# Kernel tuning notes

Measured on AMD Instinct MI355X. Metric: run time of the kernel, lower is better.

## Reference

```python
import jax, jax.numpy as jnp
import numpy as np

N, E = 10000, 320000
IN, H, C, ED = 256, 4, 64, 64
HC = H * C
EPS = 1e-5
NEG_SLOPE = 0.2


def setup_inputs() -> dict:
    key = jax.random.key(0)
    ks = jax.random.split(key, 12)
    g = lambda k, shape, fan: jax.random.normal(k, shape, jnp.float32) * (1.0 / np.sqrt(fan))
    return {
        "x": jax.random.normal(ks[0], (N, IN), jnp.float32),
        "edge_index": jax.random.randint(ks[1], (2, E), 0, N, jnp.int64),
        "edge_attr": jax.random.normal(ks[2], (E, ED), jnp.float32),
        "Wl": g(ks[3], (HC, IN), IN),   # lin_l weight (source)
        "bl": jnp.zeros((HC,), jnp.float32),
        "Wr": g(ks[4], (HC, IN), IN),   # lin_r weight (target)
        "br": jnp.zeros((HC,), jnp.float32),
        "We": g(ks[5], (HC, ED), ED),   # lin_edge weight (no bias)
        "att": g(ks[6], (H, C), C),
        "bias": jnp.zeros((HC,), jnp.float32),
        "gamma": jnp.ones((HC,), jnp.float32),
        "beta": jnp.zeros((HC,), jnp.float32),
    }


def reference(x, edge_index, edge_attr, Wl, bl, Wr, br, We, att, bias, gamma, beta):
    src, dst = edge_index[0], edge_index[1]
    # add_self_loops with fill_value='mean': loop edge_attr = mean of incoming attrs
    ones = jnp.ones((E,), jnp.float32)
    cnt = jax.ops.segment_sum(ones, dst, num_segments=N)              # [N]
    loop_attr = jax.ops.segment_sum(edge_attr, dst, num_segments=N) / jnp.maximum(cnt, 1.0)[:, None]
    node_ids = jnp.arange(N, dtype=src.dtype)
    src_f = jnp.concatenate([src, node_ids])                          # [E+N]
    dst_f = jnp.concatenate([dst, node_ids])
    ea = jnp.concatenate([edge_attr, loop_attr], axis=0)              # [E+N, ED]

    xl = (x @ Wl.T + bl).reshape(N, H, C)   # source-side projection
    xr = (x @ Wr.T + br).reshape(N, H, C)   # target-side projection
    ep = (ea @ We.T).reshape(-1, H, C)       # edge projection

    m = xl[src_f] + xr[dst_f] + ep                                    # [E+N, H, C]
    m = jnp.where(m >= 0, m, NEG_SLOPE * m)                           # leaky_relu(0.2)
    logits = jnp.einsum("ehc,hc->eh", m, att)                        # [E+N, H]

    # segment softmax over target node dst_f (every node has a self loop)
    mx = jax.ops.segment_max(logits, dst_f, num_segments=N)
    ex = jnp.exp(logits - mx[dst_f])
    den = jax.ops.segment_sum(ex, dst_f, num_segments=N)
    alpha = ex / den[dst_f]                                           # [E+N, H]

    out = jax.ops.segment_sum(xl[src_f] * alpha[:, :, None], dst_f, num_segments=N)
    h = out.reshape(N, HC) + bias

    # SiLU then LayerNorm, dropout is identity in eval
    h = h * jax.nn.sigmoid(h)
    mu = jnp.mean(h, axis=-1, keepdims=True)
    var = jnp.mean((h - mu) ** 2, axis=-1, keepdims=True)
    h = (h - mu) * jax.lax.rsqrt(var + EPS) * gamma + beta
    return h, alpha
```

## Files before the change

### kernel.cpp

```cpp
#include <hip/hip_runtime.h>

#define N_NODES 10000
#define N_EDGES 320000
#define NE_TOT  330000
#define NEG_SLOPE 0.2f
#define LN_EPS 1e-5f

#define OFF_CNT    0u
#define OFF_FILL   40000u
#define OFF_ROWPTR 80128u
#define OFF_EIDS   120320u
#define OFF_POSE   1440512u
#define OFF_XLH    4000512u
#define OFF_XRH    9120512u
#define OFF_LOG    14240512u
#define OFF_WLF    19520512u
#define OFF_WRF    19651584u
#define OFF_WEF    19782656u
#define OFF_SD     19815424u
#define OFF_EAC    21135424u

typedef __bf16 bf16x8 __attribute__((ext_vector_type(8)));
typedef float  f32x4  __attribute__((ext_vector_type(4)));
typedef unsigned short us4 __attribute__((ext_vector_type(4)));

__device__ __forceinline__ float bf2f(unsigned short u) {
    union { unsigned int i; float f; } v;
    v.i = ((unsigned int)u) << 16;
    return v.f;
}
__device__ __forceinline__ float lo2f(unsigned int u) {
    union { unsigned int i; float f; } v;
    v.i = u << 16;
    return v.f;
}
__device__ __forceinline__ float hi2f(unsigned int u) {
    union { unsigned int i; float f; } v;
    v.i = u & 0xFFFF0000u;
    return v.f;
}
__device__ __forceinline__ unsigned short f2bf(float x) {
    __bf16 b = (__bf16)x;
    return __builtin_bit_cast(unsigned short, b);
}
__device__ __forceinline__ bf16x8 cvt8(const float* p) {
    float4 v0 = *reinterpret_cast<const float4*>(p);
    float4 v1 = *reinterpret_cast<const float4*>(p + 4);
    bf16x8 t;
    t[0] = (__bf16)v0.x; t[1] = (__bf16)v0.y; t[2] = (__bf16)v0.z; t[3] = (__bf16)v0.w;
    t[4] = (__bf16)v1.x; t[5] = (__bf16)v1.y; t[6] = (__bf16)v1.z; t[7] = (__bf16)v1.w;
    return t;
}

__global__ void k_count(const int* __restrict__ ei, int* __restrict__ cnt) {
    int e = blockIdx.x * blockDim.x + threadIdx.x;
    if (e < N_EDGES) atomicAdd(&cnt[ei[N_EDGES + e]], 1);
}

__global__ void k_scan(const int* __restrict__ cnt, int* __restrict__ row_ptr) {
    __shared__ int sums[1024];
    int t = threadIdx.x;
    const int CH = 10;
    int base = t * CH;
    int s = 0;
    for (int i = 0; i < CH; i++) {
        int n = base + i;
        if (n < N_NODES) s += cnt[n] + 1;
    }
    sums[t] = s;
    __syncthreads();
    for (int off = 1; off < 1024; off <<= 1) {
        int v = (t >= off) ? sums[t - off] : 0;
        __syncthreads();
        sums[t] += v;
        __syncthreads();
    }
    int run = (t == 0) ? 0 : sums[t - 1];
    for (int i = 0; i < CH; i++) {
        int n = base + i;
        if (n < N_NODES) { row_ptr[n] = run; run += cnt[n] + 1; }
    }
    if (t == 1023) row_ptr[N_NODES] = sums[1023];
}

__global__ void k_fill(const int* __restrict__ ei, const int* __restrict__ row_ptr,
                       int* __restrict__ fill, int* __restrict__ eids,
                       int* __restrict__ sdv, int* __restrict__ pose) {
    int e = blockIdx.x * blockDim.x + threadIdx.x;
    if (e >= NE_TOT) return;
    int s, d;
    if (e < N_EDGES) { s = ei[e]; d = ei[N_EDGES + e]; }
    else             { s = e - N_EDGES; d = s; }
    int pos = atomicAdd(&fill[d], 1);
    int p = row_ptr[d] + pos;
    eids[p] = e;
    sdv[p] = s | (d << 16);
    pose[e] = p;
}

__global__ void k_permute_e(const float* __restrict__ edge_attr,
                            const int* __restrict__ pose,
                            unsigned short* __restrict__ eac) {
    int idx = blockIdx.x * blockDim.x + threadIdx.x;
    if (idx >= N_EDGES * 32) return;
    int e = idx >> 5, cp = idx & 31;
    float2 v = reinterpret_cast<const float2*>(edge_attr)[(size_t)e * 32 + cp];
    int p = pose[e];
    unsigned int u = ((unsigned int)f2bf(v.x)) | (((unsigned int)f2bf(v.y)) << 16);
    reinterpret_cast<unsigned int*>(eac)[(size_t)p * 32 + cp] = u;
}

__global__ void k_self_attr(const int* __restrict__ row_ptr,
                            const int* __restrict__ pose,
                            unsigned short* __restrict__ eac) {
    int node = (blockIdx.x << 2) + (threadIdx.x >> 6);
    int lane = threadIdx.x & 63;
    int b = row_ptr[node], en = row_ptr[node + 1];
    int selfp = pose[N_EDGES + node];
    float s0 = 0.0f, s1 = 0.0f;
    int i = b;
    for (; i + 1 < en; i += 2) {
        float a0 = bf2f(eac[(size_t)(i + 0) * 64 + lane]);
        float a1 = bf2f(eac[(size_t)(i + 1) * 64 + lane]);
        s0 += (i + 0 == selfp) ? 0.0f : a0;
        s1 += (i + 1 == selfp) ? 0.0f : a1;
    }
    for (; i < en; i++) {
        float a = bf2f(eac[(size_t)i * 64 + lane]);
        s0 += (i == selfp) ? 0.0f : a;
    }
    float s = s0 + s1;
    float c = (float)(en - b - 1);
    eac[(size_t)selfp * 64 + lane] = f2bf(s / fmaxf(c, 1.0f));
}

__global__ void k_prep_wfrag(const float* __restrict__ Wl,
                             const float* __restrict__ Wr,
                             const float* __restrict__ We,
                             unsigned short* __restrict__ wlf,
                             unsigned short* __restrict__ wrf,
                             unsigned short* __restrict__ wef) {
    int idx = blockIdx.x * 256 + threadIdx.x;
    if (idx >= 8192) return;
    int ln = idx & 63;
    int ts = (idx >> 6) & 7;
    int ct = idx >> 9;
    int c = ct * 16 + (ln & 15);
    int k0 = ts * 32 + (ln >> 4) * 8;
    *reinterpret_cast<bf16x8*>(wlf + (size_t)idx * 8) = cvt8(Wl + (size_t)c * 256 + k0);
    *reinterpret_cast<bf16x8*>(wrf + (size_t)idx * 8) = cvt8(Wr + (size_t)c * 256 + k0);
    if (idx < 2048) {
        int f = idx >> 6;
        int cb = f >> 1, step = f & 1;
        int ce = cb * 16 + (ln & 15);
        int ke = step * 32 + (ln >> 4) * 8;
        *reinterpret_cast<bf16x8*>(wef + (size_t)idx * 8) = cvt8(We + (size_t)ce * 64 + ke);
    }
}

__global__ __launch_bounds__(256) void k_gemm_mfma(
        const float* __restrict__ x,
        const float* __restrict__ bl, const float* __restrict__ br,
        const unsigned short* __restrict__ wlf,
        const unsigned short* __restrict__ wrf,
        unsigned short* __restrict__ xlh,
        unsigned short* __restrict__ xrh) {
    __shared__ __bf16 xs[8 * 64 * 8];
    int tid = threadIdx.x;
    int nb = blockIdx.x * 16;

    for (int f = tid; f < 512; f += 256) {
        int t = f >> 6, ln = f & 63;
        int node = nb + (ln & 15);
        int k0 = t * 32 + (ln >> 4) * 8;
        *reinterpret_cast<bf16x8*>(&xs[f * 8]) = cvt8(x + (size_t)node * 256 + k0);
    }
    __syncthreads();

    int lane = tid & 63;
    int wv = tid >> 6;
    int quad = lane >> 4;
    int ln15 = lane & 15;

    bf16x8 bfr[8];
#pragma unroll
    for (int t = 0; t < 8; t++)
        bfr[t] = *reinterpret_cast<const bf16x8*>(&xs[(t * 64 + lane) * 8]);

    int node = nb + ln15;
#pragma unroll
    for (int ci = 0; ci < 4; ci++) {
        int ct = wv * 4 + ci;
        f32x4 accl, accr;
        accl[0] = accl[1] = accl[2] = accl[3] = 0.0f;
        accr[0] = accr[1] = accr[2] = accr[3] = 0.0f;
#pragma unroll
        for (int t = 0; t < 8; t++) {
            bf16x8 al = *reinterpret_cast<const bf16x8*>(
                wlf + ((size_t)(ct * 8 + t) * 64 + lane) * 8);
            accl = __builtin_amdgcn_mfma_f32_16x16x32_bf16(al, bfr[t], accl, 0, 0, 0);
        }
#pragma unroll
        for (int t = 0; t < 8; t++) {
            bf16x8 ar = *reinterpret_cast<const bf16x8*>(
                wrf + ((size_t)(ct * 8 + t) * 64 + lane) * 8);
            accr = __builtin_amdgcn_mfma_f32_16x16x32_bf16(ar, bfr[t], accr, 0, 0, 0);
        }
        int cbase = ct * 16 + quad * 4;
        float4 blv = *reinterpret_cast<const float4*>(bl + cbase);
        float4 brv = *reinterpret_cast<const float4*>(br + cbase);
        us4 ol, orr;
        ol[0] = f2bf(accl[0] + blv.x); ol[1] = f2bf(accl[1] + blv.y);
        ol[2] = f2bf(accl[2] + blv.z); ol[3] = f2bf(accl[3] + blv.w);
        orr[0] = f2bf(accr[0] + brv.x); orr[1] = f2bf(accr[1] + brv.y);
        orr[2] = f2bf(accr[2] + brv.z); orr[3] = f2bf(accr[3] + brv.w);
        *reinterpret_cast<us4*>(xlh + (size_t)node * 256 + cbase) = ol;
        *reinterpret_cast<us4*>(xrh + (size_t)node * 256 + cbase) = orr;
    }
}

__global__ __launch_bounds__(256) void k_logits_v2(
        const int* __restrict__ sdv,
        const unsigned short* __restrict__ eac,
        const unsigned short* __restrict__ wef,
        const unsigned short* __restrict__ xlh,
        const unsigned short* __restrict__ xrh,
        const float* __restrict__ att,
        float* __restrict__ logits) {
    __shared__ unsigned short ep_s[4][4096];
    int tid = threadIdx.x;
    int wv = tid >> 6, lane = tid & 63;
    int h = lane >> 4, l15 = lane & 15;
    unsigned short* eps = ep_s[wv];

    const uint2* xl2 = reinterpret_cast<const uint2*>(xlh);
    const uint2* xr2 = reinterpret_cast<const uint2*>(xrh);
    float4 atv = reinterpret_cast<const float4*>(att)[lane];

    int wswz = (l15 & 3) << 4;

    const int ntiles = NE_TOT / 16;
#pragma unroll 1
    for (int t = blockIdx.x * 4 + wv; t < ntiles; t += gridDim.x * 4) {
        int pos0 = t * 16;
        int sdl = sdv[pos0 + l15];

        const unsigned short* row = eac + (size_t)(pos0 + l15) * 64;
        bf16x8 b0 = *reinterpret_cast<const bf16x8*>(row + h * 8);
        bf16x8 b1 = *reinterpret_cast<const bf16x8*>(row + 32 + h * 8);
#pragma unroll
        for (int cb = 0; cb < 16; cb++) {
            f32x4 acc;
            acc[0] = acc[1] = acc[2] = acc[3] = 0.0f;
            bf16x8 a0 = *reinterpret_cast<const bf16x8*>(
                wef + ((size_t)(cb * 2 + 0) * 64 + lane) * 8);
            bf16x8 a1 = *reinterpret_cast<const bf16x8*>(
                wef + ((size_t)(cb * 2 + 1) * 64 + lane) * 8);
            acc = __builtin_amdgcn_mfma_f32_16x16x32_bf16(a0, b0, acc, 0, 0, 0);
            acc = __builtin_amdgcn_mfma_f32_16x16x32_bf16(a1, b1, acc, 0, 0, 0);
            us4 o;
            o[0] = f2bf(acc[0]); o[1] = f2bf(acc[1]);
            o[2] = f2bf(acc[2]); o[3] = f2bf(acc[3]);
            *reinterpret_cast<us4*>(&eps[l15 * 256 + ((cb * 16 + h * 4) ^ wswz)]) = o;
        }

#pragma unroll 4
        for (int j = 0; j < 16; j++) {
            int pos = pos0 + j;
            int sd = __shfl(sdl, j, 64);
            int s = sd & 0xFFFF;
            int d = sd >> 16;
            uint2 xlv = xl2[(size_t)s * 64 + lane];
            uint2 xrv = xr2[(size_t)d * 64 + lane];
            us4 epv = *reinterpret_cast<const us4*>(
                &eps[j * 256 + ((lane * 4) ^ ((j & 3) << 4))]);
            float v0 = lo2f(xlv.x) + lo2f(xrv.x) + bf2f(epv[0]);
            v0 = fmaxf(v0, NEG_SLOPE * v0);
            float v1 = hi2f(xlv.x) + hi2f(xrv.x) + bf2f(epv[1]);
            v1 = fmaxf(v1, NEG_SLOPE * v1);
            float v2 = lo2f(xlv.y) + lo2f(xrv.y) + bf2f(epv[2]);
            v2 = fmaxf(v2, NEG_SLOPE * v2);
            float v3 = hi2f(xlv.y) + hi2f(xrv.y) + bf2f(epv[3]);
            v3 = fmaxf(v3, NEG_SLOPE * v3);
            float hs = fmaf(v0, atv.x, fmaf(v1, atv.y, fmaf(v2, atv.z, v3 * atv.w)));
            hs += __shfl_xor(hs, 1, 64);
            hs += __shfl_xor(hs, 2, 64);
            hs += __shfl_xor(hs, 4, 64);
            hs += __shfl_xor(hs, 8, 64);
            if (l15 == 0) logits[(size_t)pos * 4 + h] = hs;
        }
    }
}

__global__ void k_aggregate(const int* __restrict__ sdv,
                            const int* __restrict__ row_ptr,
                            const int* __restrict__ eids,
                            const float* __restrict__ logits,
                            const unsigned short* __restrict__ xlh,
                            const float* __restrict__ bias,
                            const float* __restrict__ gamma,
                            const float* __restrict__ beta,
                            float* __restrict__ hout,
                            float* __restrict__ alpha_out) {
    int node = (blockIdx.x << 2) + (threadIdx.x >> 6);
    int lane = threadIdx.x & 63;
    int h = lane >> 4;
    int b = row_ptr[node], en = row_ptr[node + 1];
    const uint2* xl2 = reinterpret_cast<const uint2*>(xlh);

    float m0 = -INFINITY, m1 = -INFINITY, m2 = -INFINITY, m3 = -INFINITY;
    int i = b;
    for (; i + 3 < en; i += 4) {
        m0 = fmaxf(m0, logits[(i + 0) * 4 + h]);
        m1 = fmaxf(m1, logits[(i + 1) * 4 + h]);
        m2 = fmaxf(m2, logits[(i + 2) * 4 + h]);
        m3 = fmaxf(m3, logits[(i + 3) * 4 + h]);
    }
    for (; i < en; i++) m0 = fmaxf(m0, logits[i * 4 + h]);
    float mh = fmaxf(fmaxf(m0, m1), fmaxf(m2, m3));

    float d0 = 0.0f, d1 = 0.0f, d2 = 0.0f, d3 = 0.0f;
    i = b;
    for (; i + 3 < en; i += 4) {
        d0 += __expf(logits[(i + 0) * 4 + h] - mh);
        d1 += __expf(logits[(i + 1) * 4 + h] - mh);
        d2 += __expf(logits[(i + 2) * 4 + h] - mh);
        d3 += __expf(logits[(i + 3) * 4 + h] - mh);
    }
    for (; i < en; i++) d0 += __expf(logits[i * 4 + h] - mh);
    float rden = 1.0f / ((d0 + d1) + (d2 + d3));

    float4 ac0; ac0.x = ac0.y = ac0.z = ac0.w = 0.0f;
    float4 ac1; ac1.x = ac1.y = ac1.z = ac1.w = 0.0f;
    i = b;
    for (; i + 3 < en; i += 4) {
        int sd0 = sdv[i + 0], sd1 = sdv[i + 1], sd2 = sdv[i + 2], sd3 = sdv[i + 3];
        float lg0 = logits[(i + 0) * 4 + h], lg1 = logits[(i + 1) * 4 + h];
        float lg2 = logits[(i + 2) * 4 + h], lg3 = logits[(i + 3) * 4 + h];
        int e0 = eids[i + 0], e1 = eids[i + 1], e2 = eids[i + 2], e3 = eids[i + 3];
        uint2 x0 = xl2[(size_t)(sd0 & 0xFFFF) * 64 + lane];
        uint2 x1 = xl2[(size_t)(sd1 & 0xFFFF) * 64 + lane];
        uint2 x2 = xl2[(size_t)(sd2 & 0xFFFF) * 64 + lane];
        uint2 x3 = xl2[(size_t)(sd3 & 0xFFFF) * 64 + lane];
        float al0 = __expf(lg0 - mh) * rden;
        float al1 = __expf(lg1 - mh) * rden;
        float al2 = __expf(lg2 - mh) * rden;
        float al3 = __expf(lg3 - mh) * rden;
        if ((lane & 15) == 0) {
            alpha_out[e0 * 4 + h] = al0; alpha_out[e1 * 4 + h] = al1;
            alpha_out[e2 * 4 + h] = al2; alpha_out[e3 * 4 + h] = al3;
        }
        ac0.x = fmaf(al0, lo2f(x0.x), ac0.x); ac0.y = fmaf(al0, hi2f(x0.x), ac0.y);
        ac0.z = fmaf(al0, lo2f(x0.y), ac0.z); ac0.w = fmaf(al0, hi2f(x0.y), ac0.w);
        ac1.x = fmaf(al1, lo2f(x1.x), ac1.x); ac1.y = fmaf(al1, hi2f(x1.x), ac1.y);
        ac1.z = fmaf(al1, lo2f(x1.y), ac1.z); ac1.w = fmaf(al1, hi2f(x1.y), ac1.w);
        ac0.x = fmaf(al2, lo2f(x2.x), ac0.x); ac0.y = fmaf(al2, hi2f(x2.x), ac0.y);
        ac0.z = fmaf(al2, lo2f(x2.y), ac0.z); ac0.w = fmaf(al2, hi2f(x2.y), ac0.w);
        ac1.x = fmaf(al3, lo2f(x3.x), ac1.x); ac1.y = fmaf(al3, hi2f(x3.x), ac1.y);
        ac1.z = fmaf(al3, lo2f(x3.y), ac1.z); ac1.w = fmaf(al3, hi2f(x3.y), ac1.w);
    }
    for (; i < en; i++) {
        int e = eids[i];
        int s = sdv[i] & 0xFFFF;
        float al = __expf(logits[i * 4 + h] - mh) * rden;
        if ((lane & 15) == 0) alpha_out[e * 4 + h] = al;
        uint2 xv = xl2[(size_t)s * 64 + lane];
        ac0.x = fmaf(al, lo2f(xv.x), ac0.x); ac0.y = fmaf(al, hi2f(xv.x), ac0.y);
        ac0.z = fmaf(al, lo2f(xv.y), ac0.z); ac0.w = fmaf(al, hi2f(xv.y), ac0.w);
    }
    float4 acc;
    acc.x = ac0.x + ac1.x;
    acc.y = ac0.y + ac1.y;
    acc.z = ac0.z + ac1.z;
    acc.w = ac0.w + ac1.w;

    const float4 b4 = reinterpret_cast<const float4*>(bias)[lane];
    float4 hv;
    hv.x = acc.x + b4.x; hv.y = acc.y + b4.y;
    hv.z = acc.z + b4.z; hv.w = acc.w + b4.w;
    hv.x = hv.x / (1.0f + __expf(-hv.x));
    hv.y = hv.y / (1.0f + __expf(-hv.y));
    hv.z = hv.z / (1.0f + __expf(-hv.z));
    hv.w = hv.w / (1.0f + __expf(-hv.w));
    float s1 = hv.x + hv.y + hv.z + hv.w;
    float s2 = hv.x * hv.x + hv.y * hv.y + hv.z * hv.z + hv.w * hv.w;
#pragma unroll
    for (int off = 1; off < 64; off <<= 1) {
        s1 += __shfl_xor(s1, off, 64);
        s2 += __shfl_xor(s2, off, 64);
    }
    float mu = s1 * (1.0f / 256.0f);
    float var = s2 * (1.0f / 256.0f) - mu * mu;
    float rs = rsqrtf(var + LN_EPS);
    const float4 g4 = reinterpret_cast<const float4*>(gamma)[lane];
    const float4 be4 = reinterpret_cast<const float4*>(beta)[lane];
    float4 o;
    o.x = (hv.x - mu) * rs * g4.x + be4.x;
    o.y = (hv.y - mu) * rs * g4.y + be4.y;
    o.z = (hv.z - mu) * rs * g4.z + be4.z;
    o.w = (hv.w - mu) * rs * g4.w + be4.w;
    reinterpret_cast<float4*>(hout)[node * 64 + lane] = o;
}

extern "C" void kernel_launch(void* const* d_in, const int* in_sizes, int n_in,
                              void* d_out, int out_size, void* d_ws, size_t ws_size,
                              hipStream_t stream) {
    (void)in_sizes; (void)n_in; (void)out_size; (void)ws_size;
    const float* x         = (const float*)d_in[0];
    const int*   ei        = (const int*)d_in[1];
    const float* edge_attr = (const float*)d_in[2];
    const float* Wl        = (const float*)d_in[3];
    const float* bl        = (const float*)d_in[4];
    const float* Wr        = (const float*)d_in[5];
    const float* br        = (const float*)d_in[6];
    const float* We        = (const float*)d_in[7];
    const float* att       = (const float*)d_in[8];
    const float* bias      = (const float*)d_in[9];
    const float* gamma     = (const float*)d_in[10];
    const float* beta      = (const float*)d_in[11];

    char* ws = (char*)d_ws;
    int*   cnt     = (int*)(ws + OFF_CNT);
    int*   fill    = (int*)(ws + OFF_FILL);
    int*   row_ptr = (int*)(ws + OFF_ROWPTR);
    int*   eids    = (int*)(ws + OFF_EIDS);
    int*   pose    = (int*)(ws + OFF_POSE);
    unsigned short* xlh = (unsigned short*)(ws + OFF_XLH);
    unsigned short* xrh = (unsigned short*)(ws + OFF_XRH);
    float* logits  = (float*)(ws + OFF_LOG);
    unsigned short* wlf = (unsigned short*)(ws + OFF_WLF);
    unsigned short* wrf = (unsigned short*)(ws + OFF_WRF);
    unsigned short* wef = (unsigned short*)(ws + OFF_WEF);
    int*   sdv     = (int*)(ws + OFF_SD);
    unsigned short* eac = (unsigned short*)(ws + OFF_EAC);

    float* hout      = (float*)d_out;
    float* alpha_out = (float*)d_out + N_NODES * 256;

    hipMemsetAsync(ws + OFF_CNT, 0, 2 * N_NODES * sizeof(int), stream);

    k_count<<<(N_EDGES + 255) / 256, 256, 0, stream>>>(ei, cnt);
    k_scan<<<1, 1024, 0, stream>>>(cnt, row_ptr);
    k_prep_wfrag<<<32, 256, 0, stream>>>(Wl, Wr, We, wlf, wrf, wef);
    k_fill<<<(NE_TOT + 255) / 256, 256, 0, stream>>>(ei, row_ptr, fill, eids, sdv, pose);
    k_gemm_mfma<<<N_NODES / 16, 256, 0, stream>>>(x, bl, br, wlf, wrf, xlh, xrh);
    k_permute_e<<<(N_EDGES * 32) / 256, 256, 0, stream>>>(edge_attr, pose, eac);
    k_self_attr<<<N_NODES / 4, 256, 0, stream>>>(row_ptr, pose, eac);
    k_logits_v2<<<1024, 256, 0, stream>>>(sdv, eac, wef, xlh, xrh, att, logits);
    k_aggregate<<<N_NODES / 4, 256, 0, stream>>>(sdv, row_ptr, eids, logits, xlh,
                                                 bias, gamma, beta, hout, alpha_out);
}
```

Baseline: 400.8 us.

## Fuse weight prep into count kernel, stage edge weights in LDS, unroll aggregation

Merges the weight-fragment conversion kernel into the edge-count kernel to save a launch. The logits kernel now copies the edge-projection weight fragments and attention vector into shared memory, adjusts the LDS swizzle to cut bank conflicts, and launches twice as many blocks. The aggregation loop is unrolled from 4 to 8 edges, with empty asm barriers that force the gathers to be issued before use. The larger LDS footprint (about 65KB per block) may lower occupancy of the logits kernel.

```diff
diff --git a/kernel.cpp b/kernel.cpp
--- a/kernel.cpp
+++ b/kernel.cpp
@@ -52,9 +52,33 @@
     return t;
 }
 
-__global__ void k_count(const int* __restrict__ ei, int* __restrict__ cnt) {
-    int e = blockIdx.x * blockDim.x + threadIdx.x;
-    if (e < N_EDGES) atomicAdd(&cnt[ei[N_EDGES + e]], 1);
+__global__ void k_pre(const int* __restrict__ ei, int* __restrict__ cnt,
+                      const float* __restrict__ Wl, const float* __restrict__ Wr,
+                      const float* __restrict__ We,
+                      unsigned short* __restrict__ wlf,
+                      unsigned short* __restrict__ wrf,
+                      unsigned short* __restrict__ wef) {
+    int gid = blockIdx.x * 256 + threadIdx.x;
+    if (gid < 8192) {
+        int idx = gid;
+        int ln = idx & 63;
+        int ts = (idx >> 6) & 7;
+        int ct = idx >> 9;
+        int c = ct * 16 + (ln & 15);
+        int k0 = ts * 32 + (ln >> 4) * 8;
+        *reinterpret_cast<bf16x8*>(wlf + (size_t)idx * 8) = cvt8(Wl + (size_t)c * 256 + k0);
+        *reinterpret_cast<bf16x8*>(wrf + (size_t)idx * 8) = cvt8(Wr + (size_t)c * 256 + k0);
+        if (idx < 2048) {
+            int f = idx >> 6;
+            int cb = f >> 1, step = f & 1;
+            int ce = cb * 16 + (ln & 15);
+            int ke = step * 32 + (ln >> 4) * 8;
+            *reinterpret_cast<bf16x8*>(wef + (size_t)idx * 8) = cvt8(We + (size_t)ce * 64 + ke);
+        }
+    } else {
+        int e = gid - 8192;
+        if (e < N_EDGES) atomicAdd(&cnt[ei[N_EDGES + e]], 1);
+    }
 }
 
 __global__ void k_scan(const int* __restrict__ cnt, int* __restrict__ row_ptr) {
@@ -134,30 +158,6 @@
     eac[(size_t)selfp * 64 + lane] = f2bf(s / fmaxf(c, 1.0f));
 }
 
-__global__ void k_prep_wfrag(const float* __restrict__ Wl,
-                             const float* __restrict__ Wr,
-                             const float* __restrict__ We,
-                             unsigned short* __restrict__ wlf,
-                             unsigned short* __restrict__ wrf,
-                             unsigned short* __restrict__ wef) {
-    int idx = blockIdx.x * 256 + threadIdx.x;
-    if (idx >= 8192) return;
-    int ln = idx & 63;
-    int ts = (idx >> 6) & 7;
-    int ct = idx >> 9;
-    int c = ct * 16 + (ln & 15);
-    int k0 = ts * 32 + (ln >> 4) * 8;
-    *reinterpret_cast<bf16x8*>(wlf + (size_t)idx * 8) = cvt8(Wl + (size_t)c * 256 + k0);
-    *reinterpret_cast<bf16x8*>(wrf + (size_t)idx * 8) = cvt8(Wr + (size_t)c * 256 + k0);
-    if (idx < 2048) {
-        int f = idx >> 6;
-        int cb = f >> 1, step = f & 1;
-        int ce = cb * 16 + (ln & 15);
-        int ke = step * 32 + (ln >> 4) * 8;
-        *reinterpret_cast<bf16x8*>(wef + (size_t)idx * 8) = cvt8(We + (size_t)ce * 64 + ke);
-    }
-}
-
 __global__ __launch_bounds__(256) void k_gemm_mfma(
         const float* __restrict__ x,
         const float* __restrict__ bl, const float* __restrict__ br,
@@ -219,7 +219,7 @@
     }
 }
 
-__global__ __launch_bounds__(256) void k_logits_v2(
+__global__ __launch_bounds__(256) void k_logits_v3(
         const int* __restrict__ sdv,
         const unsigned short* __restrict__ eac,
         const unsigned short* __restrict__ wef,
@@ -227,17 +227,29 @@
         const unsigned short* __restrict__ xrh,
         const float* __restrict__ att,
         float* __restrict__ logits) {
+    __shared__ __bf16 wef_s[2048 * 8];
     __shared__ unsigned short ep_s[4][4096];
+    __shared__ float att_s[256];
     int tid = threadIdx.x;
+    for (int f = tid; f < 2048; f += 256) {
+        *reinterpret_cast<bf16x8*>(&wef_s[(size_t)f * 8]) =
+            *reinterpret_cast<const bf16x8*>(wef + (size_t)f * 8);
+    }
+    if (tid < 64) {
+        reinterpret_cast<float4*>(att_s)[tid] =
+            reinterpret_cast<const float4*>(att)[tid];
+    }
+    __syncthreads();
+
     int wv = tid >> 6, lane = tid & 63;
     int h = lane >> 4, l15 = lane & 15;
     unsigned short* eps = ep_s[wv];
 
     const uint2* xl2 = reinterpret_cast<const uint2*>(xlh);
     const uint2* xr2 = reinterpret_cast<const uint2*>(xrh);
-    float4 atv = reinterpret_cast<const float4*>(att)[lane];
-
-    int wswz = (l15 & 3) << 4;
+    float4 atv = reinterpret_cast<const float4*>(att_s)[lane];
+
+    int wsw = ((l15 & 3) << 4) | ((l15 >> 2) << 2);
 
     const int ntiles = NE_TOT / 16;
 #pragma unroll 1
@@ -253,15 +265,15 @@
             f32x4 acc;
             acc[0] = acc[1] = acc[2] = acc[3] = 0.0f;
             bf16x8 a0 = *reinterpret_cast<const bf16x8*>(
-                wef + ((size_t)(cb * 2 + 0) * 64 + lane) * 8);
+                &wef_s[((size_t)(cb * 2 + 0) * 64 + lane) * 8]);
             bf16x8 a1 = *reinterpret_cast<const bf16x8*>(
-                wef + ((size_t)(cb * 2 + 1) * 64 + lane) * 8);
+                &wef_s[((size_t)(cb * 2 + 1) * 64 + lane) * 8]);
             acc = __builtin_amdgcn_mfma_f32_16x16x32_bf16(a0, b0, acc, 0, 0, 0);
             acc = __builtin_amdgcn_mfma_f32_16x16x32_bf16(a1, b1, acc, 0, 0, 0);
             us4 o;
             o[0] = f2bf(acc[0]); o[1] = f2bf(acc[1]);
             o[2] = f2bf(acc[2]); o[3] = f2bf(acc[3]);
-            *reinterpret_cast<us4*>(&eps[l15 * 256 + ((cb * 16 + h * 4) ^ wswz)]) = o;
+            *reinterpret_cast<us4*>(&eps[l15 * 256 + ((cb * 16 + h * 4) ^ wsw)]) = o;
         }
 
 #pragma unroll 4
@@ -272,8 +284,9 @@
             int d = sd >> 16;
             uint2 xlv = xl2[(size_t)s * 64 + lane];
             uint2 xrv = xr2[(size_t)d * 64 + lane];
+            int jsw = ((j & 3) << 4) | ((j >> 2) << 2);
             us4 epv = *reinterpret_cast<const us4*>(
-                &eps[j * 256 + ((lane * 4) ^ ((j & 3) << 4))]);
+                &eps[j * 256 + ((lane * 4) ^ jsw)]);
             float v0 = lo2f(xlv.x) + lo2f(xrv.x) + bf2f(epv[0]);
             v0 = fmaxf(v0, NEG_SLOPE * v0);
             float v1 = hi2f(xlv.x) + hi2f(xrv.x) + bf2f(epv[1]);
@@ -333,22 +346,41 @@
     float4 ac0; ac0.x = ac0.y = ac0.z = ac0.w = 0.0f;
     float4 ac1; ac1.x = ac1.y = ac1.z = ac1.w = 0.0f;
     i = b;
-    for (; i + 3 < en; i += 4) {
+    for (; i + 7 < en; i += 8) {
         int sd0 = sdv[i + 0], sd1 = sdv[i + 1], sd2 = sdv[i + 2], sd3 = sdv[i + 3];
+        int sd4 = sdv[i + 4], sd5 = sdv[i + 5], sd6 = sdv[i + 6], sd7 = sdv[i + 7];
         float lg0 = logits[(i + 0) * 4 + h], lg1 = logits[(i + 1) * 4 + h];
         float lg2 = logits[(i + 2) * 4 + h], lg3 = logits[(i + 3) * 4 + h];
+        float lg4 = logits[(i + 4) * 4 + h], lg5 = logits[(i + 5) * 4 + h];
+        float lg6 = logits[(i + 6) * 4 + h], lg7 = logits[(i + 7) * 4 + h];
         int e0 = eids[i + 0], e1 = eids[i + 1], e2 = eids[i + 2], e3 = eids[i + 3];
+        int e4 = eids[i + 4], e5 = eids[i + 5], e6 = eids[i + 6], e7 = eids[i + 7];
         uint2 x0 = xl2[(size_t)(sd0 & 0xFFFF) * 64 + lane];
         uint2 x1 = xl2[(size_t)(sd1 & 0xFFFF) * 64 + lane];
         uint2 x2 = xl2[(size_t)(sd2 & 0xFFFF) * 64 + lane];
         uint2 x3 = xl2[(size_t)(sd3 & 0xFFFF) * 64 + lane];
+        uint2 x4 = xl2[(size_t)(sd4 & 0xFFFF) * 64 + lane];
+        uint2 x5 = xl2[(size_t)(sd5 & 0xFFFF) * 64 + lane];
+        uint2 x6 = xl2[(size_t)(sd6 & 0xFFFF) * 64 + lane];
+        uint2 x7 = xl2[(size_t)(sd7 & 0xFFFF) * 64 + lane];
+        asm volatile("" : "+v"(x0.x), "+v"(x0.y), "+v"(x1.x), "+v"(x1.y),
+                          "+v"(x2.x), "+v"(x2.y), "+v"(x3.x), "+v"(x3.y));
+        asm volatile("" : "+v"(x4.x), "+v"(x4.y), "+v"(x5.x), "+v"(x5.y),
+                          "+v"(x6.x), "+v"(x6.y), "+v"(x7.x), "+v"(x7.y));
+
         float al0 = __expf(lg0 - mh) * rden;
         float al1 = __expf(lg1 - mh) * rden;
         float al2 = __expf(lg2 - mh) * rden;
         float al3 = __expf(lg3 - mh) * rden;
+        float al4 = __expf(lg4 - mh) * rden;
+        float al5 = __expf(lg5 - mh) * rden;
+        float al6 = __expf(lg6 - mh) * rden;
+        float al7 = __expf(lg7 - mh) * rden;
         if ((lane & 15) == 0) {
             alpha_out[e0 * 4 + h] = al0; alpha_out[e1 * 4 + h] = al1;
             alpha_out[e2 * 4 + h] = al2; alpha_out[e3 * 4 + h] = al3;
+            alpha_out[e4 * 4 + h] = al4; alpha_out[e5 * 4 + h] = al5;
+            alpha_out[e6 * 4 + h] = al6; alpha_out[e7 * 4 + h] = al7;
         }
         ac0.x = fmaf(al0, lo2f(x0.x), ac0.x); ac0.y = fmaf(al0, hi2f(x0.x), ac0.y);
         ac0.z = fmaf(al0, lo2f(x0.y), ac0.z); ac0.w = fmaf(al0, hi2f(x0.y), ac0.w);
@@ -358,6 +390,14 @@
         ac0.z = fmaf(al2, lo2f(x2.y), ac0.z); ac0.w = fmaf(al2, hi2f(x2.y), ac0.w);
         ac1.x = fmaf(al3, lo2f(x3.x), ac1.x); ac1.y = fmaf(al3, hi2f(x3.x), ac1.y);
         ac1.z = fmaf(al3, lo2f(x3.y), ac1.z); ac1.w = fmaf(al3, hi2f(x3.y), ac1.w);
+        ac0.x = fmaf(al4, lo2f(x4.x), ac0.x); ac0.y = fmaf(al4, hi2f(x4.x), ac0.y);
+        ac0.z = fmaf(al4, lo2f(x4.y), ac0.z); ac0.w = fmaf(al4, hi2f(x4.y), ac0.w);
+        ac1.x = fmaf(al5, lo2f(x5.x), ac1.x); ac1.y = fmaf(al5, hi2f(x5.x), ac1.y);
+        ac1.z = fmaf(al5, lo2f(x5.y), ac1.z); ac1.w = fmaf(al5, hi2f(x5.y), ac1.w);
+        ac0.x = fmaf(al6, lo2f(x6.x), ac0.x); ac0.y = fmaf(al6, hi2f(x6.x), ac0.y);
+        ac0.z = fmaf(al6, lo2f(x6.y), ac0.z); ac0.w = fmaf(al6, hi2f(x6.y), ac0.w);
+        ac1.x = fmaf(al7, lo2f(x7.x), ac1.x); ac1.y = fmaf(al7, hi2f(x7.x), ac1.y);
+        ac1.z = fmaf(al7, lo2f(x7.y), ac1.z); ac1.w = fmaf(al7, hi2f(x7.y), ac1.w);
     }
     for (; i < en; i++) {
         int e = eids[i];
@@ -439,14 +479,14 @@
 
     hipMemsetAsync(ws + OFF_CNT, 0, 2 * N_NODES * sizeof(int), stream);
 
-    k_count<<<(N_EDGES + 255) / 256, 256, 0, stream>>>(ei, cnt);
+    k_pre<<<(8192 + N_EDGES) / 256, 256, 0, stream>>>(ei, cnt, Wl, Wr, We,
+                                                      wlf, wrf, wef);
     k_scan<<<1, 1024, 0, stream>>>(cnt, row_ptr);
-    k_prep_wfrag<<<32, 256, 0, stream>>>(Wl, Wr, We, wlf, wrf, wef);
     k_fill<<<(NE_TOT + 255) / 256, 256, 0, stream>>>(ei, row_ptr, fill, eids, sdv, pose);
     k_gemm_mfma<<<N_NODES / 16, 256, 0, stream>>>(x, bl, br, wlf, wrf, xlh, xrh);
     k_permute_e<<<(N_EDGES * 32) / 256, 256, 0, stream>>>(edge_attr, pose, eac);
     k_self_attr<<<N_NODES / 4, 256, 0, stream>>>(row_ptr, pose, eac);
-    k_logits_v2<<<1024, 256, 0, stream>>>(sdv, eac, wef, xlh, xrh, att, logits);
+    k_logits_v3<<<2048, 256, 0, stream>>>(sdv, eac, wef, xlh, xrh, att, logits);
     k_aggregate<<<N_NODES / 4, 256, 0, stream>>>(sdv, row_ptr, eids, logits, xlh,
                                                  bias, gamma, beta, hout, alpha_out);
 }
```

Result: no change. 393.8 us (-1.7%).
